# Optimization experiments

Measured on AMD Instinct MI355X. Metric: run time of the kernel, lower is better.

Reference implementation:

```python
import jax, jax.numpy as jnp
import numpy as np

B, L, S, H, E, D = 4, 2048, 2048, 8, 64, 64

def setup_inputs() -> dict:
    key = jax.random.key(0)
    kq, kk, kv = jax.random.split(key, 3)
    queries = jax.random.normal(kq, (B, L, H, E), dtype=jnp.float32)
    keys = jax.random.normal(kk, (B, S, H, E), dtype=jnp.float32)
    values = jax.random.normal(kv, (B, S, H, D), dtype=jnp.float32)
    # TriangularCausalMask: True above the diagonal (positions to mask)
    causal = jnp.triu(jnp.ones((L, S), dtype=bool), k=1)
    attn_mask = jnp.broadcast_to(causal[None, None], (B, 1, L, S))
    return {"queries": queries, "keys": keys, "values": values, "attn_mask": attn_mask}

def reference(queries, keys, values, attn_mask):
    scale = 1.0 / jnp.sqrt(jnp.asarray(E, queries.dtype))
    # scores: [B,H,L,S]
    scores = jnp.einsum('blhe,bshe->bhls', queries, keys)
    neg_inf = jnp.asarray(-jnp.inf, scores.dtype)
    scores = jnp.where(attn_mask, neg_inf, scores)
    A = jax.nn.softmax(scale * scores, axis=-1)
    # dropout is identity in eval mode
    V = jnp.einsum('bhls,bshd->blhd', A, values)
    return V
```

## Files before the change

kernel.cpp:

```cpp
#include <hip/hip_runtime.h>
#include <math.h>

typedef __attribute__((ext_vector_type(8))) short bf16x8;
typedef __attribute__((ext_vector_type(4))) float f32x4;
typedef __attribute__((ext_vector_type(4))) unsigned int u32x4;

#define B_ 4
#define L_ 2048
#define S_ 2048
#define H_ 8
#define E_ 64
#define D_ 64
#define NT_ 32
#define TILE_BYTES 16384
#define WS_NEEDED ((size_t)B_ * H_ * NT_ * TILE_BYTES)
#define SCL (0.125f * 1.44269504088896f)

__device__ __forceinline__ unsigned short f2bf(float x) {
    unsigned int u = __builtin_bit_cast(unsigned int, x);
    u += 0x7fffu + ((u >> 16) & 1u);
    return (unsigned short)(u >> 16);
}
__device__ __forceinline__ int rho(int r) {
    return (r & 32) | (((r >> 2) & 1) << 4) | (((r >> 3) & 3) << 2) | (r & 3);
}

__global__ __launch_bounds__(256) void prep_kv(const float* __restrict__ K,
                                               const float* __restrict__ V,
                                               unsigned short* __restrict__ ws)
{
    __shared__ __align__(16) unsigned short vt[64][80];
    const int tid = threadIdx.x;
    const int bid = blockIdx.x;
    const int kt = bid & (NT_ - 1);
    const int bh = bid >> 5;
    const int b  = bh >> 3, h = bh & 7;
    const int s0 = kt * 64;
    const int r  = tid >> 2;
    const int e0 = (tid & 3) * 16;

    const float* krow = K + (((size_t)(b * S_ + s0 + r)) * H_ + h) * E_ + e0;
    const float* vrow = V + (((size_t)(b * S_ + s0 + r)) * H_ + h) * D_ + e0;
    char* tile = (char*)(ws) + ((size_t)bid * TILE_BYTES);

    unsigned short kb[16];
    #pragma unroll
    for (int i = 0; i < 4; ++i) {
        f32x4 k4 = *(const f32x4*)(krow + i * 4);
        #pragma unroll
        for (int j = 0; j < 4; ++j) kb[i * 4 + j] = f2bf(k4[j]);
    }
    {
        const int rr = rho(r);
        const int m  = (rr & 7) << 4;
        char* kbase = tile + rr * 128;
        u32x4 lo, hi;
        #pragma unroll
        for (int j = 0; j < 4; ++j) {
            lo[j] = (unsigned)kb[2 * j] | ((unsigned)kb[2 * j + 1] << 16);
            hi[j] = (unsigned)kb[8 + 2 * j] | ((unsigned)kb[9 + 2 * j] << 16);
        }
        *(u32x4*)(kbase + ((2 * e0) ^ m))      = lo;
        *(u32x4*)(kbase + ((2 * e0 + 16) ^ m)) = hi;
    }
    #pragma unroll
    for (int i = 0; i < 4; ++i) {
        f32x4 v4 = *(const f32x4*)(vrow + i * 4);
        #pragma unroll
        for (int j = 0; j < 4; ++j) vt[e0 + i * 4 + j][r] = f2bf(v4[j]);
    }
    __syncthreads();
    {
        const int d  = tid >> 2;
        const int c0 = (tid & 3) * 16;
        const int m  = (d & 7) << 4;
        char* vbase = tile + 8192 + d * 128;
        u32x4 lo = *(const u32x4*)&vt[d][c0];
        u32x4 hi = *(const u32x4*)&vt[d][c0 + 8];
        *(u32x4*)(vbase + ((2 * c0) ^ m))      = lo;
        *(u32x4*)(vbase + ((2 * c0 + 16) ^ m)) = hi;
    }
}

#define GL16(dst, p, o) asm volatile("global_load_dwordx4 %0, %1, off offset:" o \
                                     : "=v"(dst) : "v"(p) : "memory")

__global__ __launch_bounds__(256, 2) void attn5(const float* __restrict__ Q,
                                                const unsigned short* __restrict__ ws,
                                                float* __restrict__ O)
{
    const int tid  = threadIdx.x;
    const int lane = tid & 63;
    const int w    = tid >> 6;
    const int lq   = lane & 15;
    const int g    = lane >> 4;

    const int bid = blockIdx.x;
    const int bh  = bid & 31;
    const int j   = bid >> 5;
    const int b0  = bh >> 3, h = bh & 7;

    const int qt = (w & 2) ? (62 - 2 * j + (w & 1)) : (2 * j + (w & 1));
    const int nt = (qt >> 1) + 1;
    int qrow[2];
    qrow[0] = qt * 32 + lq;
    qrow[1] = qt * 32 + 16 + lq;

    bf16x8 qf[2][2];
    #pragma unroll
    for (int qs = 0; qs < 2; ++qs) {
        const float* qptr = Q + (((size_t)(b0 * L_ + qrow[qs])) * H_ + h) * E_;
        #pragma unroll
        for (int eb = 0; eb < 2; ++eb) {
            const float* pq = qptr + eb * 32 + g * 8;
            f32x4 a = *(const f32x4*)pq;
            f32x4 b = *(const f32x4*)(pq + 4);
            bf16x8 qv;
            #pragma unroll
            for (int k = 0; k < 4; ++k) {
                qv[k]     = (short)f2bf(a[k] * SCL);
                qv[4 + k] = (short)f2bf(b[k] * SCL);
            }
            qf[qs][eb] = qv;
        }
    }

    const char* tb = (const char*)ws + (size_t)bh * NT_ * TILE_BYTES;
    const int mm  = (lq & 7) << 4;
    const int o_a = lq * 128 + ((16 * g) ^ mm) + 3072;
    const int o_b = lq * 128 + ((64 + 16 * g) ^ mm) + 3072;
    const char* pKa = tb + o_a;
    const char* pKb = tb + o_b;
    const char* pVa = tb + 8192 + o_a;
    const char* pVb = tb + 8192 + o_b;

    u32x4 ka[8], vb[8];
    f32x4 acc[2][4] = {};
    float ls[2] = {0.f, 0.f};

    GL16(ka[0], pKa, "-3072"); GL16(ka[1], pKb, "-3072");
    GL16(ka[2], pKa, "-1024"); GL16(ka[3], pKb, "-1024");
    GL16(ka[4], pKa, "1024");  GL16(ka[5], pKb, "1024");
    GL16(ka[6], pKa, "3072");  GL16(ka[7], pKb, "3072");
    GL16(vb[0], pVa, "-3072"); GL16(vb[1], pVb, "-3072");
    GL16(vb[2], pVa, "-1024"); GL16(vb[3], pVb, "-1024");
    GL16(vb[4], pVa, "1024");  GL16(vb[5], pVb, "1024");
    GL16(vb[6], pVa, "3072");  GL16(vb[7], pVb, "3072");

    for (int kt = 0; kt < nt; ++kt) {
        const bool notlast = (kt + 1 < nt);

        asm volatile("s_waitcnt vmcnt(8)" ::: "memory");
        __builtin_amdgcn_sched_barrier(0);

        f32x4 sc[2][4];
        __builtin_amdgcn_s_setprio(1);
        #pragma unroll
        for (int st = 0; st < 4; ++st) {
            bf16x8 ka0 = __builtin_bit_cast(bf16x8, ka[2 * st]);
            bf16x8 ka1 = __builtin_bit_cast(bf16x8, ka[2 * st + 1]);
            #pragma unroll
            for (int qs = 0; qs < 2; ++qs) {
                f32x4 z = {0.f, 0.f, 0.f, 0.f};
                f32x4 c = __builtin_amdgcn_mfma_f32_16x16x32_bf16(ka0, qf[qs][0], z, 0, 0, 0);
                sc[qs][st] = __builtin_amdgcn_mfma_f32_16x16x32_bf16(ka1, qf[qs][1], c, 0, 0, 0);
            }
        }
        __builtin_amdgcn_s_setprio(0);

        if (notlast) {
            pKa += TILE_BYTES; pKb += TILE_BYTES;
            GL16(ka[0], pKa, "-3072"); GL16(ka[1], pKb, "-3072");
            GL16(ka[2], pKa, "-1024"); GL16(ka[3], pKb, "-1024");
            GL16(ka[4], pKa, "1024");  GL16(ka[5], pKb, "1024");
            GL16(ka[6], pKa, "3072");  GL16(ka[7], pKb, "3072");
        }

        const int kv0 = kt * 64;
        u32x4 pw[2][2];
        #pragma unroll
        for (int qs = 0; qs < 2; ++qs) {
            #pragma unroll
            for (int st = 0; st < 4; ++st) {
                f32x4 c = sc[qs][st];
                if (kt == nt - 1) {
                    #pragma unroll
                    for (int r = 0; r < 4; ++r) {
                        const int kv = kv0 + 32 * (st >> 1) + 8 * g + 4 * (st & 1) + r;
                        if (kv > qrow[qs]) c[r] = -INFINITY;
                    }
                }
                f32x4 ev;
                #pragma unroll
                for (int r = 0; r < 4; ++r)
                    asm("v_exp_f32 %0, %1" : "=v"(ev[r]) : "v"(c[r]));
                ls[qs] += (ev[0] + ev[1]) + (ev[2] + ev[3]);
                asm("v_cvt_pk_bf16_f32 %0, %1, %2" : "=v"(pw[qs][st >> 1][2 * (st & 1)])     : "v"(ev[0]), "v"(ev[1]));
                asm("v_cvt_pk_bf16_f32 %0, %1, %2" : "=v"(pw[qs][st >> 1][2 * (st & 1) + 1]) : "v"(ev[2]), "v"(ev[3]));
            }
        }

        if (notlast) asm volatile("s_waitcnt vmcnt(8)" ::: "memory");
        else         asm volatile("s_waitcnt vmcnt(0)" ::: "memory");
        __builtin_amdgcn_sched_barrier(0);

        __builtin_amdgcn_s_setprio(1);
        #pragma unroll
        for (int dt = 0; dt < 4; ++dt) {
            bf16x8 va0 = __builtin_bit_cast(bf16x8, vb[2 * dt]);
            bf16x8 va1 = __builtin_bit_cast(bf16x8, vb[2 * dt + 1]);
            #pragma unroll
            for (int qs = 0; qs < 2; ++qs) {
                acc[qs][dt] = __builtin_amdgcn_mfma_f32_16x16x32_bf16(va0, __builtin_bit_cast(bf16x8, pw[qs][0]), acc[qs][dt], 0, 0, 0);
                acc[qs][dt] = __builtin_amdgcn_mfma_f32_16x16x32_bf16(va1, __builtin_bit_cast(bf16x8, pw[qs][1]), acc[qs][dt], 0, 0, 0);
            }
        }
        __builtin_amdgcn_s_setprio(0);

        if (notlast) {
            pVa += TILE_BYTES; pVb += TILE_BYTES;
            GL16(vb[0], pVa, "-3072"); GL16(vb[1], pVb, "-3072");
            GL16(vb[2], pVa, "-1024"); GL16(vb[3], pVb, "-1024");
            GL16(vb[4], pVa, "1024");  GL16(vb[5], pVb, "1024");
            GL16(vb[6], pVa, "3072");  GL16(vb[7], pVb, "3072");
        }
    }

    #pragma unroll
    for (int qs = 0; qs < 2; ++qs) {
        float l = ls[qs] + __shfl_xor(ls[qs], 16);
        l += __shfl_xor(l, 32);
        const float inv = 1.0f / l;
        float* op = O + (((size_t)(b0 * L_ + qrow[qs])) * H_ + h) * D_;
        #pragma unroll
        for (int dt = 0; dt < 4; ++dt) {
            f32x4 o;
            #pragma unroll
            for (int r = 0; r < 4; ++r) o[r] = acc[qs][dt][r] * inv;
            *(f32x4*)(op + dt * 16 + 4 * g) = o;
        }
    }
}

#define KPITCH 72
__global__ __launch_bounds__(256, 2) void attn_fwd_fb(
    const float* __restrict__ Q, const float* __restrict__ K,
    const float* __restrict__ V, float* __restrict__ O)
{
    __shared__ unsigned short Klds[64 * KPITCH];
    __shared__ unsigned short Vlds[64 * KPITCH];
    const int tid = threadIdx.x, lane = tid & 63, w = tid >> 6;
    const int lq = lane & 15, g = lane >> 4;
    const int bid = blockIdx.x, qb = bid & 31, bh = bid >> 5;
    const int b0 = bh >> 3, h = bh & 7;
    const int q0 = qb * 64, qrow = q0 + w * 16 + lq;
    const float* qptr = Q + ((size_t)(b0 * L_ + qrow) * H_ + h) * E_;
    bf16x8 qf[2];
    #pragma unroll
    for (int eb = 0; eb < 2; ++eb) {
        const float* p = qptr + eb * 32 + g * 8;
        f32x4 a = *(const f32x4*)p; f32x4 b = *(const f32x4*)(p + 4);
        bf16x8 q;
        #pragma unroll
        for (int jq = 0; jq < 4; ++jq) { q[jq] = (short)f2bf(a[jq] * 0.125f); q[4 + jq] = (short)f2bf(b[jq] * 0.125f); }
        qf[eb] = q;
    }
    const int tr = tid >> 2, tc = tid & 3;
    const int rh = rho(tr);
    f32x4 acc[4] = {};
    float mrow = -INFINITY, lrow = 0.f;
    for (int kt = 0; kt < qb + 1; ++kt) {
        const int kv0 = kt * 64;
        __syncthreads();
        {
            const float* krow = K + ((size_t)((b0 * S_ + kv0 + tr)) * H_ + h) * E_;
            const float* vrow = V + ((size_t)((b0 * S_ + kv0 + tr)) * H_ + h) * D_;
            #pragma unroll
            for (int i = 0; i < 4; ++i) {
                const int e0 = tc * 4 + i * 16;
                f32x4 k4 = *(const f32x4*)(krow + e0);
                unsigned int lo = (unsigned)f2bf(k4[0]) | ((unsigned)f2bf(k4[1]) << 16);
                unsigned int hi = (unsigned)f2bf(k4[2]) | ((unsigned)f2bf(k4[3]) << 16);
                *(uint2*)&Klds[rh * KPITCH + e0] = make_uint2(lo, hi);
                f32x4 v4 = *(const f32x4*)(vrow + e0);
                #pragma unroll
                for (int k2 = 0; k2 < 4; ++k2) Vlds[(e0 + k2) * KPITCH + tr] = f2bf(v4[k2]);
            }
        }
        __syncthreads();
        f32x4 sc[4];
        #pragma unroll
        for (int st = 0; st < 4; ++st) {
            const unsigned short* kr = &Klds[(st * 16 + lq) * KPITCH];
            bf16x8 ka0 = *(const bf16x8*)(kr + 8 * g);
            bf16x8 ka1 = *(const bf16x8*)(kr + 32 + 8 * g);
            f32x4 c = {0.f, 0.f, 0.f, 0.f};
            c = __builtin_amdgcn_mfma_f32_16x16x32_bf16(ka0, qf[0], c, 0, 0, 0);
            c = __builtin_amdgcn_mfma_f32_16x16x32_bf16(ka1, qf[1], c, 0, 0, 0);
            sc[st] = c;
        }
        float tmax = -INFINITY;
        #pragma unroll
        for (int st = 0; st < 4; ++st) {
            const int kvb = kv0 + 32 * (st >> 1) + 8 * g + 4 * (st & 1);
            #pragma unroll
            for (int r = 0; r < 4; ++r) { if (kvb + r > qrow) sc[st][r] = -INFINITY; tmax = fmaxf(tmax, sc[st][r]); }
        }
        tmax = fmaxf(tmax, __shfl_xor(tmax, 16));
        tmax = fmaxf(tmax, __shfl_xor(tmax, 32));
        const float mnew = fmaxf(mrow, tmax);
        const float corr = __expf(mrow - mnew);
        float p[4][4]; float tsum = 0.f;
        #pragma unroll
        for (int st = 0; st < 4; ++st)
            #pragma unroll
            for (int r = 0; r < 4; ++r) { float e = __expf(sc[st][r] - mnew); p[st][r] = e; tsum += e; }
        tsum += __shfl_xor(tsum, 16); tsum += __shfl_xor(tsum, 32);
        lrow = lrow * corr + tsum; mrow = mnew;
        #pragma unroll
        for (int dt = 0; dt < 4; ++dt)
            #pragma unroll
            for (int r = 0; r < 4; ++r) acc[dt][r] *= corr;
        bf16x8 pb[2];
        #pragma unroll
        for (int bb = 0; bb < 2; ++bb)
            #pragma unroll
            for (int s = 0; s < 2; ++s)
                #pragma unroll
                for (int r = 0; r < 4; ++r) pb[bb][4 * s + r] = (short)f2bf(p[2 * bb + s][r]);
        #pragma unroll
        for (int bb = 0; bb < 2; ++bb)
            #pragma unroll
            for (int dt = 0; dt < 4; ++dt) {
                bf16x8 va = *(const bf16x8*)&Vlds[(dt * 16 + lq) * KPITCH + 32 * bb + 8 * g];
                acc[dt] = __builtin_amdgcn_mfma_f32_16x16x32_bf16(va, pb[bb], acc[dt], 0, 0, 0);
            }
    }
    const float inv = 1.0f / lrow;
    float* optr = O + ((size_t)(b0 * L_ + qrow) * H_ + h) * D_;
    #pragma unroll
    for (int dt = 0; dt < 4; ++dt) {
        f32x4 o;
        #pragma unroll
        for (int r = 0; r < 4; ++r) o[r] = acc[dt][r] * inv;
        *(f32x4*)(optr + dt * 16 + 4 * g) = o;
    }
}

extern "C" void kernel_launch(void* const* d_in, const int* in_sizes, int n_in,
                              void* d_out, int out_size, void* d_ws, size_t ws_size,
                              hipStream_t stream) {
    const float* Q = (const float*)d_in[0];
    const float* K = (const float*)d_in[1];
    const float* V = (const float*)d_in[2];
    float* O = (float*)d_out;
    if (ws_size >= WS_NEEDED) {
        prep_kv<<<dim3(B_ * H_ * NT_), 256, 0, stream>>>(K, V, (unsigned short*)d_ws);
        attn5<<<dim3(512), 256, 0, stream>>>(Q, (const unsigned short*)d_ws, O);
    } else {
        attn_fwd_fb<<<dim3(B_ * H_ * 32), 256, 0, stream>>>(Q, K, V, O);
    }
}
```

Before: 46.11 us.

## Split KV range of paired causal query tiles across waves with LDS reduction

The attention kernel now pairs a short query tile p with its long mirror 63-p and splits the combined KV range evenly between two waves. One wave handles all of tile A plus the first part of tile B, and the other handles the rest of tile B. Partial numerators and row sums are merged through shared-memory atomics and normalized in an epilogue. This balances causal work across waves within a block. In exchange it adds LDS atomics, an extra sync, extra Q loads, and a larger shared-memory footprint.

```diff
diff --git a/kernel.cpp b/kernel.cpp
--- a/kernel.cpp
+++ b/kernel.cpp
@@ -48,7 +48,7 @@
     for (int i = 0; i < 4; ++i) {
         f32x4 k4 = *(const f32x4*)(krow + i * 4);
         #pragma unroll
-        for (int j = 0; j < 4; ++j) kb[i * 4 + j] = f2bf(k4[j]);
+        for (int jq = 0; jq < 4; ++jq) kb[i * 4 + jq] = f2bf(k4[jq]);
     }
     {
         const int rr = rho(r);
@@ -56,9 +56,9 @@
         char* kbase = tile + rr * 128;
         u32x4 lo, hi;
         #pragma unroll
-        for (int j = 0; j < 4; ++j) {
-            lo[j] = (unsigned)kb[2 * j] | ((unsigned)kb[2 * j + 1] << 16);
-            hi[j] = (unsigned)kb[8 + 2 * j] | ((unsigned)kb[9 + 2 * j] << 16);
+        for (int jq = 0; jq < 4; ++jq) {
+            lo[jq] = (unsigned)kb[2 * jq] | ((unsigned)kb[2 * jq + 1] << 16);
+            hi[jq] = (unsigned)kb[8 + 2 * jq] | ((unsigned)kb[9 + 2 * jq] << 16);
         }
         *(u32x4*)(kbase + ((2 * e0) ^ m))      = lo;
         *(u32x4*)(kbase + ((2 * e0 + 16) ^ m)) = hi;
@@ -67,7 +67,7 @@
     for (int i = 0; i < 4; ++i) {
         f32x4 v4 = *(const f32x4*)(vrow + i * 4);
         #pragma unroll
-        for (int j = 0; j < 4; ++j) vt[e0 + i * 4 + j][r] = f2bf(v4[j]);
+        for (int jq = 0; jq < 4; ++jq) vt[e0 + i * 4 + jq][r] = f2bf(v4[jq]);
     }
     __syncthreads();
     {
@@ -83,12 +83,146 @@
 }
 
 #define GL16(dst, p, o) asm volatile("global_load_dwordx4 %0, %1, off offset:" o \
-                                     : "=v"(dst) : "v"(p) : "memory")
-
-__global__ __launch_bounds__(256, 2) void attn5(const float* __restrict__ Q,
+                                     : "=&v"(dst) : "v"(p) : "memory")
+
+#define ISSUE_K() do { \
+    GL16(ka[0], pKa, "-3072"); GL16(ka[1], pKb, "-3072"); \
+    GL16(ka[2], pKa, "-1024"); GL16(ka[3], pKb, "-1024"); \
+    GL16(ka[4], pKa, "1024");  GL16(ka[5], pKb, "1024");  \
+    GL16(ka[6], pKa, "3072");  GL16(ka[7], pKb, "3072"); } while (0)
+
+#define ISSUE_V() do { \
+    GL16(vb[0], pVa, "-3072"); GL16(vb[1], pVb, "-3072"); \
+    GL16(vb[2], pVa, "-1024"); GL16(vb[3], pVb, "-1024"); \
+    GL16(vb[4], pVa, "1024");  GL16(vb[5], pVb, "1024");  \
+    GL16(vb[6], pVa, "3072");  GL16(vb[7], pVb, "3072"); } while (0)
+
+__device__ __forceinline__ void do_range(
+    const float* __restrict__ Q, const char* __restrict__ tb,
+    int b0, int h, int qt, int kv_from, int kv_to, int diag_kt,
+    int lq, int g, float (*LaccS)[66], float* LlS)
+{
+    if (kv_from >= kv_to) return;
+    int qrow[2];
+    qrow[0] = qt * 32 + lq;
+    qrow[1] = qt * 32 + 16 + lq;
+
+    bf16x8 qf[2][2];
+    #pragma unroll
+    for (int qs = 0; qs < 2; ++qs) {
+        const float* qptr = Q + (((size_t)(b0 * L_ + qrow[qs])) * H_ + h) * E_;
+        #pragma unroll
+        for (int eb = 0; eb < 2; ++eb) {
+            const float* pq = qptr + eb * 32 + g * 8;
+            f32x4 a = *(const f32x4*)pq;
+            f32x4 b = *(const f32x4*)(pq + 4);
+            bf16x8 qv;
+            #pragma unroll
+            for (int k = 0; k < 4; ++k) {
+                qv[k]     = (short)f2bf(a[k] * SCL);
+                qv[4 + k] = (short)f2bf(b[k] * SCL);
+            }
+            qf[qs][eb] = qv;
+        }
+    }
+
+    const int mm  = (lq & 7) << 4;
+    const char* pKa = tb + (size_t)kv_from * TILE_BYTES + lq * 128 + ((16 * g) ^ mm) + 3072;
+    const char* pKb = tb + (size_t)kv_from * TILE_BYTES + lq * 128 + (((64 + 16 * g)) ^ mm) + 3072;
+    const char* pVa = pKa + 8192;
+    const char* pVb = pKb + 8192;
+
+    u32x4 ka[8], vb[8];
+    f32x4 acc[2][4] = {};
+    float ls[2] = {0.f, 0.f};
+
+    ISSUE_K();
+    ISSUE_V();
+
+    for (int kt = kv_from; kt < kv_to; ++kt) {
+        asm volatile("s_waitcnt vmcnt(8)" ::: "memory");
+        __builtin_amdgcn_sched_barrier(0);
+
+        f32x4 sc[2][4];
+        __builtin_amdgcn_s_setprio(1);
+        #pragma unroll
+        for (int st = 0; st < 4; ++st) {
+            bf16x8 k0 = __builtin_bit_cast(bf16x8, ka[2 * st]);
+            bf16x8 k1 = __builtin_bit_cast(bf16x8, ka[2 * st + 1]);
+            #pragma unroll
+            for (int qs = 0; qs < 2; ++qs) {
+                f32x4 z = {0.f, 0.f, 0.f, 0.f};
+                f32x4 cc = __builtin_amdgcn_mfma_f32_16x16x32_bf16(k0, qf[qs][0], z, 0, 0, 0);
+                sc[qs][st] = __builtin_amdgcn_mfma_f32_16x16x32_bf16(k1, qf[qs][1], cc, 0, 0, 0);
+            }
+        }
+        __builtin_amdgcn_s_setprio(0);
+
+        const bool hasnext = (kt + 1 < kv_to);
+        if (hasnext) { pKa += TILE_BYTES; pKb += TILE_BYTES; ISSUE_K(); }
+
+        const int kv0 = kt * 64;
+        u32x4 pw[2][2];
+        #pragma unroll
+        for (int qs = 0; qs < 2; ++qs) {
+            #pragma unroll
+            for (int st = 0; st < 4; ++st) {
+                f32x4 cc = sc[qs][st];
+                if (kt == diag_kt) {
+                    #pragma unroll
+                    for (int r = 0; r < 4; ++r) {
+                        const int kv = kv0 + 32 * (st >> 1) + 8 * g + 4 * (st & 1) + r;
+                        if (kv > qrow[qs]) cc[r] = -INFINITY;
+                    }
+                }
+                f32x4 ev;
+                #pragma unroll
+                for (int r = 0; r < 4; ++r)
+                    asm("v_exp_f32 %0, %1" : "=v"(ev[r]) : "v"(cc[r]));
+                ls[qs] += (ev[0] + ev[1]) + (ev[2] + ev[3]);
+                asm("v_cvt_pk_bf16_f32 %0, %1, %2" : "=v"(pw[qs][st >> 1][2 * (st & 1)])     : "v"(ev[0]), "v"(ev[1]));
+                asm("v_cvt_pk_bf16_f32 %0, %1, %2" : "=v"(pw[qs][st >> 1][2 * (st & 1) + 1]) : "v"(ev[2]), "v"(ev[3]));
+            }
+        }
+
+        if (hasnext) asm volatile("s_waitcnt vmcnt(8)" ::: "memory");
+        else         asm volatile("s_waitcnt vmcnt(0)" ::: "memory");
+        __builtin_amdgcn_sched_barrier(0);
+
+        __builtin_amdgcn_s_setprio(1);
+        #pragma unroll
+        for (int dt = 0; dt < 4; ++dt) {
+            bf16x8 v0 = __builtin_bit_cast(bf16x8, vb[2 * dt]);
+            bf16x8 v1 = __builtin_bit_cast(bf16x8, vb[2 * dt + 1]);
+            #pragma unroll
+            for (int qs = 0; qs < 2; ++qs) {
+                acc[qs][dt] = __builtin_amdgcn_mfma_f32_16x16x32_bf16(v0, __builtin_bit_cast(bf16x8, pw[qs][0]), acc[qs][dt], 0, 0, 0);
+                acc[qs][dt] = __builtin_amdgcn_mfma_f32_16x16x32_bf16(v1, __builtin_bit_cast(bf16x8, pw[qs][1]), acc[qs][dt], 0, 0, 0);
+            }
+        }
+        __builtin_amdgcn_s_setprio(0);
+
+        if (hasnext) { pVa += TILE_BYTES; pVb += TILE_BYTES; ISSUE_V(); }
+    }
+
+    #pragma unroll
+    for (int qs = 0; qs < 2; ++qs) {
+        #pragma unroll
+        for (int dt = 0; dt < 4; ++dt)
+            #pragma unroll
+            for (int r = 0; r < 4; ++r)
+                atomicAdd(&LaccS[qs * 16 + lq][dt * 16 + 4 * g + r], acc[qs][dt][r]);
+        atomicAdd(&LlS[qs * 16 + lq], ls[qs]);
+    }
+}
+
+__global__ __launch_bounds__(256, 2) void attn7(const float* __restrict__ Q,
                                                 const unsigned short* __restrict__ ws,
                                                 float* __restrict__ O)
 {
+    __shared__ float Lacc[4][32][66];
+    __shared__ float Ll[4][32];
+
     const int tid  = threadIdx.x;
     const int lane = tid & 63;
     const int w    = tid >> 6;
@@ -100,145 +234,41 @@
     const int j   = bid >> 5;
     const int b0  = bh >> 3, h = bh & 7;
 
-    const int qt = (w & 2) ? (62 - 2 * j + (w & 1)) : (2 * j + (w & 1));
-    const int nt = (qt >> 1) + 1;
-    int qrow[2];
-    qrow[0] = qt * 32 + lq;
-    qrow[1] = qt * 32 + 16 + lq;
-
-    bf16x8 qf[2][2];
-    #pragma unroll
-    for (int qs = 0; qs < 2; ++qs) {
-        const float* qptr = Q + (((size_t)(b0 * L_ + qrow[qs])) * H_ + h) * E_;
-        #pragma unroll
-        for (int eb = 0; eb < 2; ++eb) {
-            const float* pq = qptr + eb * 32 + g * 8;
-            f32x4 a = *(const f32x4*)pq;
-            f32x4 b = *(const f32x4*)(pq + 4);
-            bf16x8 qv;
-            #pragma unroll
-            for (int k = 0; k < 4; ++k) {
-                qv[k]     = (short)f2bf(a[k] * SCL);
-                qv[4 + k] = (short)f2bf(b[k] * SCL);
-            }
-            qf[qs][eb] = qv;
-        }
-    }
+    const int pi = w >> 1;
+    const int c  = w & 1;
+    const int p  = pi ? (j + 16) : j;
+    const int qtA = p, qtB = 63 - p;
+    const int ntA = (p >> 1) + 1;
+    const int ntB = ((63 - p) >> 1) + 1;
+
+    for (int i = tid; i < 4 * 32 * 66; i += 256) ((float*)Lacc)[i] = 0.f;
+    if (tid < 128) ((float*)Ll)[tid] = 0.f;
+    __syncthreads();
 
     const char* tb = (const char*)ws + (size_t)bh * NT_ * TILE_BYTES;
-    const int mm  = (lq & 7) << 4;
-    const int o_a = lq * 128 + ((16 * g) ^ mm) + 3072;
-    const int o_b = lq * 128 + ((64 + 16 * g) ^ mm) + 3072;
-    const char* pKa = tb + o_a;
-    const char* pKb = tb + o_b;
-    const char* pVa = tb + 8192 + o_a;
-    const char* pVb = tb + 8192 + o_b;
-
-    u32x4 ka[8], vb[8];
-    f32x4 acc[2][4] = {};
-    float ls[2] = {0.f, 0.f};
-
-    GL16(ka[0], pKa, "-3072"); GL16(ka[1], pKb, "-3072");
-    GL16(ka[2], pKa, "-1024"); GL16(ka[3], pKb, "-1024");
-    GL16(ka[4], pKa, "1024");  GL16(ka[5], pKb, "1024");
-    GL16(ka[6], pKa, "3072");  GL16(ka[7], pKb, "3072");
-    GL16(vb[0], pVa, "-3072"); GL16(vb[1], pVb, "-3072");
-    GL16(vb[2], pVa, "-1024"); GL16(vb[3], pVb, "-1024");
-    GL16(vb[4], pVa, "1024");  GL16(vb[5], pVb, "1024");
-    GL16(vb[6], pVa, "3072");  GL16(vb[7], pVb, "3072");
-
-    for (int kt = 0; kt < nt; ++kt) {
-        const bool notlast = (kt + 1 < nt);
-
-        asm volatile("s_waitcnt vmcnt(8)" ::: "memory");
-        __builtin_amdgcn_sched_barrier(0);
-
-        f32x4 sc[2][4];
-        __builtin_amdgcn_s_setprio(1);
-        #pragma unroll
-        for (int st = 0; st < 4; ++st) {
-            bf16x8 ka0 = __builtin_bit_cast(bf16x8, ka[2 * st]);
-            bf16x8 ka1 = __builtin_bit_cast(bf16x8, ka[2 * st + 1]);
-            #pragma unroll
-            for (int qs = 0; qs < 2; ++qs) {
-                f32x4 z = {0.f, 0.f, 0.f, 0.f};
-                f32x4 c = __builtin_amdgcn_mfma_f32_16x16x32_bf16(ka0, qf[qs][0], z, 0, 0, 0);
-                sc[qs][st] = __builtin_amdgcn_mfma_f32_16x16x32_bf16(ka1, qf[qs][1], c, 0, 0, 0);
-            }
-        }
-        __builtin_amdgcn_s_setprio(0);
-
-        if (notlast) {
-            pKa += TILE_BYTES; pKb += TILE_BYTES;
-            GL16(ka[0], pKa, "-3072"); GL16(ka[1], pKb, "-3072");
-            GL16(ka[2], pKa, "-1024"); GL16(ka[3], pKb, "-1024");
-            GL16(ka[4], pKa, "1024");  GL16(ka[5], pKb, "1024");
-            GL16(ka[6], pKa, "3072");  GL16(ka[7], pKb, "3072");
-        }
-
-        const int kv0 = kt * 64;
-        u32x4 pw[2][2];
-        #pragma unroll
-        for (int qs = 0; qs < 2; ++qs) {
-            #pragma unroll
-            for (int st = 0; st < 4; ++st) {
-                f32x4 c = sc[qs][st];
-                if (kt == nt - 1) {
-                    #pragma unroll
-                    for (int r = 0; r < 4; ++r) {
-                        const int kv = kv0 + 32 * (st >> 1) + 8 * g + 4 * (st & 1) + r;
-                        if (kv > qrow[qs]) c[r] = -INFINITY;
-                    }
-                }
-                f32x4 ev;
-                #pragma unroll
-                for (int r = 0; r < 4; ++r)
-                    asm("v_exp_f32 %0, %1" : "=v"(ev[r]) : "v"(c[r]));
-                ls[qs] += (ev[0] + ev[1]) + (ev[2] + ev[3]);
-                asm("v_cvt_pk_bf16_f32 %0, %1, %2" : "=v"(pw[qs][st >> 1][2 * (st & 1)])     : "v"(ev[0]), "v"(ev[1]));
-                asm("v_cvt_pk_bf16_f32 %0, %1, %2" : "=v"(pw[qs][st >> 1][2 * (st & 1) + 1]) : "v"(ev[2]), "v"(ev[3]));
-            }
-        }
-
-        if (notlast) asm volatile("s_waitcnt vmcnt(8)" ::: "memory");
-        else         asm volatile("s_waitcnt vmcnt(0)" ::: "memory");
-        __builtin_amdgcn_sched_barrier(0);
-
-        __builtin_amdgcn_s_setprio(1);
-        #pragma unroll
-        for (int dt = 0; dt < 4; ++dt) {
-            bf16x8 va0 = __builtin_bit_cast(bf16x8, vb[2 * dt]);
-            bf16x8 va1 = __builtin_bit_cast(bf16x8, vb[2 * dt + 1]);
-            #pragma unroll
-            for (int qs = 0; qs < 2; ++qs) {
-                acc[qs][dt] = __builtin_amdgcn_mfma_f32_16x16x32_bf16(va0, __builtin_bit_cast(bf16x8, pw[qs][0]), acc[qs][dt], 0, 0, 0);
-                acc[qs][dt] = __builtin_amdgcn_mfma_f32_16x16x32_bf16(va1, __builtin_bit_cast(bf16x8, pw[qs][1]), acc[qs][dt], 0, 0, 0);
-            }
-        }
-        __builtin_amdgcn_s_setprio(0);
-
-        if (notlast) {
-            pVa += TILE_BYTES; pVb += TILE_BYTES;
-            GL16(vb[0], pVa, "-3072"); GL16(vb[1], pVb, "-3072");
-            GL16(vb[2], pVa, "-1024"); GL16(vb[3], pVb, "-1024");
-            GL16(vb[4], pVa, "1024");  GL16(vb[5], pVb, "1024");
-            GL16(vb[6], pVa, "3072");  GL16(vb[7], pVb, "3072");
-        }
-    }
-
-    #pragma unroll
-    for (int qs = 0; qs < 2; ++qs) {
-        float l = ls[qs] + __shfl_xor(ls[qs], 16);
-        l += __shfl_xor(l, 32);
-        const float inv = 1.0f / l;
-        float* op = O + (((size_t)(b0 * L_ + qrow[qs])) * H_ + h) * D_;
-        #pragma unroll
-        for (int dt = 0; dt < 4; ++dt) {
-            f32x4 o;
-            #pragma unroll
-            for (int r = 0; r < 4; ++r) o[r] = acc[qs][dt][r] * inv;
-            *(f32x4*)(op + dt * 16 + 4 * g) = o;
-        }
+
+    if (c == 0) {
+        do_range(Q, tb, b0, h, qtA, 0, ntA, ntA - 1, lq, g, Lacc[pi * 2 + 0], Ll[pi * 2 + 0]);
+        do_range(Q, tb, b0, h, qtB, 0, 16 - ntA, ntB - 1, lq, g, Lacc[pi * 2 + 1], Ll[pi * 2 + 1]);
+    } else {
+        do_range(Q, tb, b0, h, qtB, 16 - ntA, ntB, ntB - 1, lq, g, Lacc[pi * 2 + 1], Ll[pi * 2 + 1]);
+    }
+
+    __syncthreads();
+
+    const int slot = tid >> 6;
+    const int row  = (tid >> 1) & 31;
+    const int d0   = (tid & 1) * 32;
+    const int pE   = (slot >> 1) ? (j + 16) : j;
+    const int qtE  = (slot & 1) ? (63 - pE) : pE;
+    const float inv = 1.0f / Ll[slot][row];
+    float* op = O + (((size_t)(b0 * L_ + qtE * 32 + row)) * H_ + h) * D_ + d0;
+    #pragma unroll
+    for (int i8 = 0; i8 < 8; ++i8) {
+        f32x4 o;
+        #pragma unroll
+        for (int r = 0; r < 4; ++r) o[r] = Lacc[slot][row][d0 + i8 * 4 + r] * inv;
+        *(f32x4*)(op + i8 * 4) = o;
     }
 }
 
@@ -258,8 +288,8 @@
     bf16x8 qf[2];
     #pragma unroll
     for (int eb = 0; eb < 2; ++eb) {
-        const float* p = qptr + eb * 32 + g * 8;
-        f32x4 a = *(const f32x4*)p; f32x4 b = *(const f32x4*)(p + 4);
+        const float* pp = qptr + eb * 32 + g * 8;
+        f32x4 a = *(const f32x4*)pp; f32x4 b = *(const f32x4*)(pp + 4);
         bf16x8 q;
         #pragma unroll
         for (int jq = 0; jq < 4; ++jq) { q[jq] = (short)f2bf(a[jq] * 0.125f); q[4 + jq] = (short)f2bf(b[jq] * 0.125f); }
@@ -294,10 +324,10 @@
             const unsigned short* kr = &Klds[(st * 16 + lq) * KPITCH];
             bf16x8 ka0 = *(const bf16x8*)(kr + 8 * g);
             bf16x8 ka1 = *(const bf16x8*)(kr + 32 + 8 * g);
-            f32x4 c = {0.f, 0.f, 0.f, 0.f};
-            c = __builtin_amdgcn_mfma_f32_16x16x32_bf16(ka0, qf[0], c, 0, 0, 0);
-            c = __builtin_amdgcn_mfma_f32_16x16x32_bf16(ka1, qf[1], c, 0, 0, 0);
-            sc[st] = c;
+            f32x4 cc = {0.f, 0.f, 0.f, 0.f};
+            cc = __builtin_amdgcn_mfma_f32_16x16x32_bf16(ka0, qf[0], cc, 0, 0, 0);
+            cc = __builtin_amdgcn_mfma_f32_16x16x32_bf16(ka1, qf[1], cc, 0, 0, 0);
+            sc[st] = cc;
         }
         float tmax = -INFINITY;
         #pragma unroll
@@ -310,11 +340,11 @@
         tmax = fmaxf(tmax, __shfl_xor(tmax, 32));
         const float mnew = fmaxf(mrow, tmax);
         const float corr = __expf(mrow - mnew);
-        float p[4][4]; float tsum = 0.f;
+        float pv[4][4]; float tsum = 0.f;
         #pragma unroll
         for (int st = 0; st < 4; ++st)
             #pragma unroll
-            for (int r = 0; r < 4; ++r) { float e = __expf(sc[st][r] - mnew); p[st][r] = e; tsum += e; }
+            for (int r = 0; r < 4; ++r) { float e = __expf(sc[st][r] - mnew); pv[st][r] = e; tsum += e; }
         tsum += __shfl_xor(tsum, 16); tsum += __shfl_xor(tsum, 32);
         lrow = lrow * corr + tsum; mrow = mnew;
         #pragma unroll
@@ -327,7 +357,7 @@
             #pragma unroll
             for (int s = 0; s < 2; ++s)
                 #pragma unroll
-                for (int r = 0; r < 4; ++r) pb[bb][4 * s + r] = (short)f2bf(p[2 * bb + s][r]);
+                for (int r = 0; r < 4; ++r) pb[bb][4 * s + r] = (short)f2bf(pv[2 * bb + s][r]);
         #pragma unroll
         for (int bb = 0; bb < 2; ++bb)
             #pragma unroll
@@ -356,7 +386,7 @@
     float* O = (float*)d_out;
     if (ws_size >= WS_NEEDED) {
         prep_kv<<<dim3(B_ * H_ * NT_), 256, 0, stream>>>(K, V, (unsigned short*)d_ws);
-        attn5<<<dim3(512), 256, 0, stream>>>(Q, (const unsigned short*)d_ws, O);
+        attn7<<<dim3(512), 256, 0, stream>>>(Q, (const unsigned short*)d_ws, O);
     } else {
         attn_fwd_fb<<<dim3(B_ * H_ * 32), 256, 0, stream>>>(Q, K, V, O);
     }
```

Result: slower. 66.47 us (+44.2%).
